# Performance work log

Hardware: AMD Instinct MI355X
Metric: run time of the kernel (lower is better)

The kernel has to match this reference:

```python
import jax, jax.numpy as jnp
import numpy as np

N = 4096        # nodes
D = 512         # in_dim = hidden_dim
E = 131072      # edges (avg degree 32)
K = 3           # aggregate_range
ALPHA = 2.0


def prelu(x, a):
    return jnp.where(x >= 0, x, a * x)


def setup_inputs() -> dict:
    key = jax.random.key(0)
    ks = jax.random.split(key, 8)
    s = 1.0 / np.sqrt(D)  # ~xavier scale
    return {
        "coeffs": jax.random.normal(ks[0], (N, D), jnp.float32),
        "edge_index": jax.random.randint(ks[1], (2, E), 0, N, dtype=jnp.int32),
        "W0": jax.random.normal(ks[2], (D, D), jnp.float32) * s,
        "b0": jnp.zeros((D,), jnp.float32),
        "a0": jnp.full((1,), 0.25, jnp.float32),
        "W1": jax.random.normal(ks[3], (D, D), jnp.float32) * s,  # use_bias=False
        "a1": jnp.full((1,), 0.25, jnp.float32),
        "W2": jax.random.normal(ks[4], (D, D), jnp.float32) * s,
        "a2": jnp.full((1,), 0.25, jnp.float32),
        "Wo": jax.random.normal(ks[5], (1, D), jnp.float32) * s,
        "bo": jnp.zeros((1,), jnp.float32),
    }


def _mlp(coeffs, W0, b0, a0, W1, a1, W2, a2, Wo, bo):
    # Linear+PReLU, then n_hidden_layers x [Linear(no bias)+PReLU+(Dropout: eval, no-op)], then Linear
    x = prelu(coeffs @ W0.T + b0, a0)
    x = prelu(x @ W1.T, a1)
    x = prelu(x @ W2.T, a2)
    return x @ Wo.T + bo  # [N, 1]


def _aggregate_k_hop(edge_index, angles):
    # Faithful to the torch code: enhanced_angles aliases angles, so each hop
    # reads the CURRENT (already enhanced) values:  a <- a + w_k * A_k @ a.
    # Hop 1 uses raw edge list (duplicate edges add twice). Hops >= 2 use
    # np.unique-deduplicated composed paths == boolean adjacency powers.
    src, dst = edge_index[0], edge_index[1]
    a = angles
    a = a + (0.5 ** ALPHA) * jax.ops.segment_sum(a[dst], src, num_segments=N)
    A = jnp.zeros((N, N), jnp.float32).at[src, dst].set(1.0)  # dedup'd boolean adjacency
    Ak = A
    for k_ in range(K - 1):
        Ak = ((Ak @ A) > 0).astype(jnp.float32)  # unique k-hop paths
        a = a + (1.0 / (k_ + 3)) ** ALPHA * (Ak @ a)
    return a


def reference(coeffs, edge_index, W0, b0, a0, W1, a1, W2, a2, Wo, bo):
    angles = _mlp(coeffs, W0, b0, a0, W1, a1, W2, a2, Wo, bo)
    return _aggregate_k_hop(edge_index, angles)
```

## Files before the change

### kernel.cpp

```cpp
#include <hip/hip_runtime.h>

#define N_NODES 4096
#define D_DIM   512
#define E_EDGES 131072
#define NWORDS  128

typedef __bf16 bf16;
typedef __bf16 bf16x4 __attribute__((ext_vector_type(4)));
typedef __bf16 bf16x8 __attribute__((ext_vector_type(8)));
typedef float  f32x4  __attribute__((ext_vector_type(4)));
typedef unsigned int u32;

#define GLOAD_LDS16(gp, lp) \
    __builtin_amdgcn_global_load_lds((const __attribute__((address_space(1))) u32*)(gp), \
                                     (__attribute__((address_space(3))) u32*)(lp), 16, 0, 0)

static const size_t OFF_W1B = 0;
static const size_t OFF_W2B = OFF_W1B + (size_t)D_DIM*D_DIM*2;
static const size_t OFF_X1  = OFF_W2B + (size_t)D_DIM*D_DIM*2;
static const size_t OFF_X2  = OFF_X1  + (size_t)N_NODES*D_DIM*2;
static const size_t OFF_ANG = OFF_X2  + (size_t)N_NODES*D_DIM*2;
static const size_t OFF_H1  = OFF_ANG + N_NODES*4;
static const size_t OFF_A2V = OFF_H1  + N_NODES*4;
static const size_t OFF_TP  = OFF_A2V + N_NODES*4;
static const size_t OFF_AB  = OFF_TP  + 1024*4;
static const size_t OFF_A2B = OFF_AB  + (size_t)N_NODES*NWORDS*4;
static const size_t OFF_A3B = OFF_A2B + (size_t)N_NODES*NWORDS*4;

__device__ __forceinline__ bf16x8 cvt8(float4 lo, float4 hi) {
    bf16x8 r;
    r[0] = (bf16)lo.x; r[1] = (bf16)lo.y; r[2] = (bf16)lo.z; r[3] = (bf16)lo.w;
    r[4] = (bf16)hi.x; r[5] = (bf16)hi.y; r[6] = (bf16)hi.z; r[7] = (bf16)hi.w;
    return r;
}

template<int MODE>
__global__ __launch_bounds__(256)
void gemm_fused(const float* __restrict__ Xf, const float* __restrict__ Wf,
                const bf16* __restrict__ X, const bf16* __restrict__ W,
                bf16* __restrict__ outB,
                const float* __restrict__ bias, const float* __restrict__ slope,
                const float* __restrict__ Wo, float* __restrict__ ang,
                const float* __restrict__ bo, float* __restrict__ h1,
                const float* __restrict__ W1f, const float* __restrict__ W2f,
                bf16* __restrict__ W1b, bf16* __restrict__ W2b,
                const int* __restrict__ esrc, const int* __restrict__ edst,
                u32* __restrict__ AbOut,
                const u32* __restrict__ P, const u32* __restrict__ Q, u32* __restrict__ BOut)
{
    __shared__ bf16 At[2][64][64];
    __shared__ bf16 Bt[2][64][64];
    __shared__ int  s_cnt[4];
    __shared__ int  s_list[4][256];
    const int bx = blockIdx.x;
    const int t = threadIdx.x;
    const int wave = t >> 6, lane = t & 63;

    if (bx < 512) {
        const int wm = wave >> 1, wn = wave & 1;
        const int quad = lane >> 4, lq = lane & 15;
        const int rowBase = (bx >> 3) * 64;
        const int colBase = (bx & 7) * 64;
        const int c0 = t, c1 = t + 256;
        const int r0 = c0 >> 3, o0 = (c0 & 7) * 8;
        const int r1 = c1 >> 3, o1 = (c1 & 7) * 8;

        f32x4 acc[2][2] = {};
        int cur = 0;

        if (MODE == 0) {
            const float* gA0 = Xf + (size_t)(rowBase + r0) * D_DIM + o0;
            const float* gA1 = Xf + (size_t)(rowBase + r1) * D_DIM + o1;
            const float* gB0 = Wf + (size_t)(colBase + r0) * D_DIM + o0;
            const float* gB1 = Wf + (size_t)(colBase + r1) * D_DIM + o1;
            float4 pa0l = *(const float4*)(gA0),     pa0h = *(const float4*)(gA0 + 4);
            float4 pa1l = *(const float4*)(gA1),     pa1h = *(const float4*)(gA1 + 4);
            float4 pb0l = *(const float4*)(gB0),     pb0h = *(const float4*)(gB0 + 4);
            float4 pb1l = *(const float4*)(gB1),     pb1h = *(const float4*)(gB1 + 4);
            for (int k0 = 0; k0 < D_DIM; k0 += 64) {
                *(bf16x8*)&At[cur][r0][o0] = cvt8(pa0l, pa0h);
                *(bf16x8*)&At[cur][r1][o1] = cvt8(pa1l, pa1h);
                *(bf16x8*)&Bt[cur][r0][o0] = cvt8(pb0l, pb0h);
                *(bf16x8*)&Bt[cur][r1][o1] = cvt8(pb1l, pb1h);
                if (k0 + 64 < D_DIM) {
                    pa0l = *(const float4*)(gA0 + k0 + 64); pa0h = *(const float4*)(gA0 + k0 + 68);
                    pa1l = *(const float4*)(gA1 + k0 + 64); pa1h = *(const float4*)(gA1 + k0 + 68);
                    pb0l = *(const float4*)(gB0 + k0 + 64); pb0h = *(const float4*)(gB0 + k0 + 68);
                    pb1l = *(const float4*)(gB1 + k0 + 64); pb1h = *(const float4*)(gB1 + k0 + 68);
                }
                __syncthreads();
                #pragma unroll
                for (int kc = 0; kc < 2; ++kc) {
                    bf16x8 af[2], bfr[2];
                    #pragma unroll
                    for (int tm = 0; tm < 2; ++tm) af[tm]  = *(const bf16x8*)&At[cur][wm * 32 + tm * 16 + lq][kc * 32 + quad * 8];
                    #pragma unroll
                    for (int tn = 0; tn < 2; ++tn) bfr[tn] = *(const bf16x8*)&Bt[cur][wn * 32 + tn * 16 + lq][kc * 32 + quad * 8];
                    #pragma unroll
                    for (int tm = 0; tm < 2; ++tm)
                        #pragma unroll
                        for (int tn = 0; tn < 2; ++tn)
                            acc[tm][tn] = __builtin_amdgcn_mfma_f32_16x16x32_bf16(af[tm], bfr[tn], acc[tm][tn], 0, 0, 0);
                }
                cur ^= 1;
            }
        } else {
            const bf16* gA0 = X + (size_t)(rowBase + r0) * D_DIM + o0;
            const bf16* gA1 = X + (size_t)(rowBase + r1) * D_DIM + o1;
            const bf16* gB0 = W + (size_t)(colBase + r0) * D_DIM + o0;
            const bf16* gB1 = W + (size_t)(colBase + r1) * D_DIM + o1;
            char* baseA = (char*)&At[0][0][0];
            char* baseB = (char*)&Bt[0][0][0];
            GLOAD_LDS16(gA0, baseA + wave * 1024);
            GLOAD_LDS16(gA1, baseA + 4096 + wave * 1024);
            GLOAD_LDS16(gB0, baseB + wave * 1024);
            GLOAD_LDS16(gB1, baseB + 4096 + wave * 1024);
            for (int k0 = 0; k0 < D_DIM; k0 += 64) {
                __syncthreads();
                if (k0 + 64 < D_DIM) {
                    int nb = (cur ^ 1) * 8192;
                    GLOAD_LDS16(gA0 + k0 + 64, baseA + nb + wave * 1024);
                    GLOAD_LDS16(gA1 + k0 + 64, baseA + nb + 4096 + wave * 1024);
                    GLOAD_LDS16(gB0 + k0 + 64, baseB + nb + wave * 1024);
                    GLOAD_LDS16(gB1 + k0 + 64, baseB + nb + 4096 + wave * 1024);
                }
                #pragma unroll
                for (int kc = 0; kc < 2; ++kc) {
                    bf16x8 af[2], bfr[2];
                    #pragma unroll
                    for (int tm = 0; tm < 2; ++tm) af[tm]  = *(const bf16x8*)&At[cur][wm * 32 + tm * 16 + lq][kc * 32 + quad * 8];
                    #pragma unroll
                    for (int tn = 0; tn < 2; ++tn) bfr[tn] = *(const bf16x8*)&Bt[cur][wn * 32 + tn * 16 + lq][kc * 32 + quad * 8];
                    #pragma unroll
                    for (int tm = 0; tm < 2; ++tm)
                        #pragma unroll
                        for (int tn = 0; tn < 2; ++tn)
                            acc[tm][tn] = __builtin_amdgcn_mfma_f32_16x16x32_bf16(af[tm], bfr[tn], acc[tm][tn], 0, 0, 0);
                }
                cur ^= 1;
            }
        }

        const float a = slope[0];
        if (MODE == 2) {
            float wo[2];
            #pragma unroll
            for (int tn = 0; tn < 2; ++tn) wo[tn] = Wo[colBase + wn * 32 + tn * 16 + lq];
            #pragma unroll
            for (int tm = 0; tm < 2; ++tm) {
                #pragma unroll
                for (int r = 0; r < 4; ++r) {
                    float p = 0.f;
                    #pragma unroll
                    for (int tn = 0; tn < 2; ++tn) {
                        float v = acc[tm][tn][r];
                        v = (v >= 0.f) ? v : a * v;
                        p += v * wo[tn];
                    }
                    #pragma unroll
                    for (int m = 1; m < 16; m <<= 1) p += __shfl_xor(p, m, 64);
                    if (lq == 0)
                        atomicAdd(&ang[rowBase + wm * 32 + tm * 16 + quad * 4 + r], p);
                }
            }
        } else {
            #pragma unroll
            for (int tm = 0; tm < 2; ++tm) {
                #pragma unroll
                for (int tn = 0; tn < 2; ++tn) {
                    int col = colBase + wn * 32 + tn * 16 + lq;
                    float b = (MODE == 0) ? bias[col] : 0.f;
                    #pragma unroll
                    for (int r = 0; r < 4; ++r) {
                        int row = rowBase + wm * 32 + tm * 16 + quad * 4 + r;
                        float v = acc[tm][tn][r] + b;
                        v = (v >= 0.f) ? v : a * v;
                        outB[(size_t)row * D_DIM + col] = (bf16)v;
                    }
                }
            }
        }
    } else if (MODE == 0) {
        if (bx < 640) {
            int base = (bx - 512) * 256 + t;
            for (int e = base; e < E_EDGES; e += 128 * 256) {
                int r = esrc[e], c = edst[e];
                atomicOr(&AbOut[(size_t)r * NWORDS + (c >> 5)], 1u << (c & 31));
            }
        } else if (bx < 768) {
            int cb = bx - 640;
            const float* src = (cb < 64) ? W1f : W2f;
            bf16* dst = (cb < 64) ? W1b : W2b;
            size_t base = (size_t)(cb & 63) * 4096;
            #pragma unroll
            for (int i = 0; i < 4; ++i) {
                size_t e = base + (size_t)(i * 256 + t) * 4;
                float4 v = *(const float4*)(src + e);
                bf16x4 o; o.x = (bf16)v.x; o.y = (bf16)v.y; o.z = (bf16)v.z; o.w = (bf16)v.w;
                *(bf16x4*)(dst + e) = o;
            }
        } else {
            float b = bo[0];
            for (int i = t; i < N_NODES; i += 256) { ang[i] = b; h1[i] = 0.f; }
        }
    } else {
        int row = (bx - 512) * 4 + wave;
        if (lane == 0) s_cnt[wave] = 0;
        __syncthreads();
        const u32* prow = P + (size_t)row * NWORDS;
        #pragma unroll
        for (int h = 0; h < 2; ++h) {
            u32 bits = prow[h * 64 + lane];
            int base = (h * 64 + lane) * 32;
            while (bits) {
                int b = __ffs(bits) - 1; bits &= bits - 1;
                int pos = atomicAdd(&s_cnt[wave], 1);
                if (pos < 256) s_list[wave][pos] = base + b;
            }
        }
        __syncthreads();
        int cnt = min(s_cnt[wave], 256);
        u32 acc0 = 0, acc1 = 0;
        int j = 0;
        for (; j + 4 <= cnt; j += 4) {
            int i0 = s_list[wave][j], i1 = s_list[wave][j + 1];
            int i2 = s_list[wave][j + 2], i3 = s_list[wave][j + 3];
            const u32* q0 = Q + (size_t)i0 * NWORDS;
            const u32* q1 = Q + (size_t)i1 * NWORDS;
            const u32* q2 = Q + (size_t)i2 * NWORDS;
            const u32* q3 = Q + (size_t)i3 * NWORDS;
            u32 x0 = q0[lane], x1 = q1[lane], x2 = q2[lane], x3 = q3[lane];
            u32 y0 = q0[64 + lane], y1 = q1[64 + lane], y2 = q2[64 + lane], y3 = q3[64 + lane];
            acc0 |= x0 | x1 | x2 | x3;
            acc1 |= y0 | y1 | y2 | y3;
        }
        for (; j < cnt; ++j) {
            const u32* q = Q + (size_t)s_list[wave][j] * NWORDS;
            acc0 |= q[lane]; acc1 |= q[64 + lane];
        }
        BOut[(size_t)row * NWORDS + lane]      = acc0;
        BOut[(size_t)row * NWORDS + 64 + lane] = acc1;
    }
}

__global__ __launch_bounds__(256)
void hop1_edges(const int* __restrict__ src, const int* __restrict__ dst,
                const float* __restrict__ ang, float* __restrict__ h1)
{
    int e = blockIdx.x * 256 + threadIdx.x;
    if (e < E_EDGES) atomicAdd(&h1[src[e]], 0.25f * ang[dst[e]]);
}

__global__ __launch_bounds__(256)
void bits_matvec2(const u32* __restrict__ A2, const float* __restrict__ ang,
                  const float* __restrict__ h1, float* __restrict__ a2,
                  float* __restrict__ Tpart)
{
    __shared__ float s_red[4];
    int wave = threadIdx.x >> 6, lane = threadIdx.x & 63;
    int row  = blockIdx.x * 4 + wave;
    float s = 0.f;
    #pragma unroll
    for (int h = 0; h < 2; ++h) {
        u32 bits = A2[(size_t)row * NWORDS + h * 64 + lane];
        int base = (h * 64 + lane) * 32;
        while (bits) {
            int b = __ffs(bits) - 1;
            bits &= bits - 1;
            s += ang[base + b] + h1[base + b];
        }
    }
    #pragma unroll
    for (int off = 32; off > 0; off >>= 1) s += __shfl_down(s, off, 64);
    if (lane == 0) {
        float val = (ang[row] + h1[row]) + (1.f / 9.f) * s;
        a2[row] = val;
        s_red[wave] = val;
    }
    __syncthreads();
    if (threadIdx.x == 0)
        Tpart[blockIdx.x] = s_red[0] + s_red[1] + s_red[2] + s_red[3];
}

__global__ __launch_bounds__(256)
void bits_matvec3(const u32* __restrict__ A3, const float* __restrict__ a2,
                  const float* __restrict__ Tpart, float* __restrict__ out)
{
    __shared__ float s_part[4];
    int wave = threadIdx.x >> 6, lane = threadIdx.x & 63;

    float tsum = 0.f;
    #pragma unroll
    for (int i = 0; i < 4; ++i) tsum += Tpart[i * 256 + threadIdx.x];
    #pragma unroll
    for (int off = 32; off > 0; off >>= 1) tsum += __shfl_down(tsum, off, 64);
    if (lane == 0) s_part[wave] = tsum;
    __syncthreads();
    const float T = s_part[0] + s_part[1] + s_part[2] + s_part[3];

    int row = blockIdx.x * 4 + wave;
    float s = 0.f;
    #pragma unroll
    for (int h = 0; h < 2; ++h) {
        u32 bits = ~A3[(size_t)row * NWORDS + h * 64 + lane];
        int base = (h * 64 + lane) * 32;
        while (bits) {
            int b = __ffs(bits) - 1;
            bits &= bits - 1;
            s += a2[base + b];
        }
    }
    #pragma unroll
    for (int off = 32; off > 0; off >>= 1) s += __shfl_down(s, off, 64);
    if (lane == 0) out[row] = a2[row] + (1.f / 16.f) * (T - s);
}

extern "C" void kernel_launch(void* const* d_in, const int* in_sizes, int n_in,
                              void* d_out, int out_size, void* d_ws, size_t ws_size,
                              hipStream_t stream) {
    const float* coeffs = (const float*)d_in[0];
    const int*   edges  = (const int*)d_in[1];
    const float* W0     = (const float*)d_in[2];
    const float* b0     = (const float*)d_in[3];
    const float* pa0    = (const float*)d_in[4];
    const float* W1     = (const float*)d_in[5];
    const float* pa1    = (const float*)d_in[6];
    const float* W2     = (const float*)d_in[7];
    const float* pa2    = (const float*)d_in[8];
    const float* Wo     = (const float*)d_in[9];
    const float* bo     = (const float*)d_in[10];
    float* out = (float*)d_out;

    char* ws = (char*)d_ws;
    bf16*  W1b  = (bf16*)(ws + OFF_W1B);
    bf16*  W2b  = (bf16*)(ws + OFF_W2B);
    bf16*  x1b  = (bf16*)(ws + OFF_X1);
    bf16*  x2b  = (bf16*)(ws + OFF_X2);
    float* ang  = (float*)(ws + OFF_ANG);
    float* h1   = (float*)(ws + OFF_H1);
    float* a2v  = (float*)(ws + OFF_A2V);
    float* Tp   = (float*)(ws + OFF_TP);
    u32*   Ab   = (u32*)(ws + OFF_AB);
    u32*   A2b  = (u32*)(ws + OFF_A2B);
    u32*   A3b  = (u32*)(ws + OFF_A3B);

    const int* srcp = edges;
    const int* dstp = edges + E_EDGES;

    hipMemsetAsync(Ab, 0, (size_t)N_NODES * NWORDS * 4, stream);

    gemm_fused<0><<<769, 256, 0, stream>>>(coeffs, W0, nullptr, nullptr, x1b, b0, pa0,
                                           nullptr, ang, bo, h1, W1, W2, W1b, W2b,
                                           srcp, dstp, Ab, nullptr, nullptr, nullptr);
    gemm_fused<1><<<1536, 256, 0, stream>>>(nullptr, nullptr, x1b, W1b, x2b, nullptr, pa1,
                                            nullptr, nullptr, nullptr, nullptr, nullptr, nullptr,
                                            nullptr, nullptr, nullptr, nullptr, nullptr, Ab, Ab, A2b);
    gemm_fused<2><<<1536, 256, 0, stream>>>(nullptr, nullptr, x2b, W2b, nullptr, nullptr, pa2,
                                            Wo, ang, nullptr, nullptr, nullptr, nullptr, nullptr, nullptr,
                                            nullptr, nullptr, nullptr, Ab, A2b, A3b);

    hop1_edges<<<E_EDGES / 256, 256, 0, stream>>>(srcp, dstp, ang, h1);
    bits_matvec2<<<N_NODES / 4, 256, 0, stream>>>(A2b, ang, h1, a2v, Tp);
    bits_matvec3<<<N_NODES / 4, 256, 0, stream>>>(A3b, a2v, Tp, out);
}
```

Baseline: 146.8 us.

## Fuse hop1 and two bitmask matvecs into one kernel with grid barriers

Replaces the three small aggregation kernels (edge atomics, hop-2 and hop-3 bit matvecs) with a single persistent kernel of 1024 blocks that separates the phases with software grid barriers built on atomic counters. The barrier counters are zeroed by the existing memset, which is extended to cover them. The goal is to remove two kernel launch gaps and their tail effects. The cost is spin-wait barrier latency, and the kernel relies on all 1024 blocks being resident at once to avoid deadlock.

```diff
diff --git a/kernel.cpp b/kernel.cpp
--- a/kernel.cpp
+++ b/kernel.cpp
@@ -4,6 +4,7 @@
 #define D_DIM   512
 #define E_EDGES 131072
 #define NWORDS  128
+#define AGG_BLOCKS 1024
 
 typedef __bf16 bf16;
 typedef __bf16 bf16x4 __attribute__((ext_vector_type(4)));
@@ -23,7 +24,9 @@
 static const size_t OFF_H1  = OFF_ANG + N_NODES*4;
 static const size_t OFF_A2V = OFF_H1  + N_NODES*4;
 static const size_t OFF_TP  = OFF_A2V + N_NODES*4;
-static const size_t OFF_AB  = OFF_TP  + 1024*4;
+static const size_t OFF_CTR = OFF_TP  + 1024*4;
+static const size_t OFF_AB  = OFF_CTR + 256;
+static const size_t ZERO_BYTES = 256 + (size_t)N_NODES*NWORDS*4;
 static const size_t OFF_A2B = OFF_AB  + (size_t)N_NODES*NWORDS*4;
 static const size_t OFF_A3B = OFF_A2B + (size_t)N_NODES*NWORDS*4;
 
@@ -32,6 +35,19 @@
     r[0] = (bf16)lo.x; r[1] = (bf16)lo.y; r[2] = (bf16)lo.z; r[3] = (bf16)lo.w;
     r[4] = (bf16)hi.x; r[5] = (bf16)hi.y; r[6] = (bf16)hi.z; r[7] = (bf16)hi.w;
     return r;
+}
+
+__device__ __forceinline__ void grid_barrier(u32* cnt) {
+    __syncthreads();
+    if (threadIdx.x == 0) {
+        __threadfence();
+        u32 arrived = atomicAdd(cnt, 1u) + 1;
+        while (arrived < AGG_BLOCKS) {
+            __builtin_amdgcn_s_sleep(1);
+            arrived = atomicAdd(cnt, 0u);
+        }
+    }
+    __syncthreads();
 }
 
 template<int MODE>
@@ -244,75 +260,73 @@
 }
 
 __global__ __launch_bounds__(256)
-void hop1_edges(const int* __restrict__ src, const int* __restrict__ dst,
-                const float* __restrict__ ang, float* __restrict__ h1)
-{
-    int e = blockIdx.x * 256 + threadIdx.x;
-    if (e < E_EDGES) atomicAdd(&h1[src[e]], 0.25f * ang[dst[e]]);
-}
-
-__global__ __launch_bounds__(256)
-void bits_matvec2(const u32* __restrict__ A2, const float* __restrict__ ang,
-                  const float* __restrict__ h1, float* __restrict__ a2,
-                  float* __restrict__ Tpart)
+void aggregate(const int* __restrict__ esrc, const int* __restrict__ edst,
+               const float* __restrict__ ang, float* __restrict__ h1,
+               const u32* __restrict__ A2, const u32* __restrict__ A3,
+               float* __restrict__ a2v, float* __restrict__ Tp,
+               u32* __restrict__ ctr, float* __restrict__ out)
 {
     __shared__ float s_red[4];
-    int wave = threadIdx.x >> 6, lane = threadIdx.x & 63;
-    int row  = blockIdx.x * 4 + wave;
-    float s = 0.f;
-    #pragma unroll
-    for (int h = 0; h < 2; ++h) {
-        u32 bits = A2[(size_t)row * NWORDS + h * 64 + lane];
-        int base = (h * 64 + lane) * 32;
-        while (bits) {
-            int b = __ffs(bits) - 1;
-            bits &= bits - 1;
-            s += ang[base + b] + h1[base + b];
-        }
-    }
-    #pragma unroll
-    for (int off = 32; off > 0; off >>= 1) s += __shfl_down(s, off, 64);
-    if (lane == 0) {
-        float val = (ang[row] + h1[row]) + (1.f / 9.f) * s;
-        a2[row] = val;
-        s_red[wave] = val;
-    }
-    __syncthreads();
-    if (threadIdx.x == 0)
-        Tpart[blockIdx.x] = s_red[0] + s_red[1] + s_red[2] + s_red[3];
-}
-
-__global__ __launch_bounds__(256)
-void bits_matvec3(const u32* __restrict__ A3, const float* __restrict__ a2,
-                  const float* __restrict__ Tpart, float* __restrict__ out)
-{
-    __shared__ float s_part[4];
-    int wave = threadIdx.x >> 6, lane = threadIdx.x & 63;
-
-    float tsum = 0.f;
-    #pragma unroll
-    for (int i = 0; i < 4; ++i) tsum += Tpart[i * 256 + threadIdx.x];
-    #pragma unroll
-    for (int off = 32; off > 0; off >>= 1) tsum += __shfl_down(tsum, off, 64);
-    if (lane == 0) s_part[wave] = tsum;
-    __syncthreads();
-    const float T = s_part[0] + s_part[1] + s_part[2] + s_part[3];
-
-    int row = blockIdx.x * 4 + wave;
-    float s = 0.f;
-    #pragma unroll
-    for (int h = 0; h < 2; ++h) {
-        u32 bits = ~A3[(size_t)row * NWORDS + h * 64 + lane];
-        int base = (h * 64 + lane) * 32;
-        while (bits) {
-            int b = __ffs(bits) - 1;
-            bits &= bits - 1;
-            s += a2[base + b];
-        }
-    }
-    #pragma unroll
-    for (int off = 32; off > 0; off >>= 1) s += __shfl_down(s, off, 64);
-    if (lane == 0) out[row] = a2[row] + (1.f / 16.f) * (T - s);
+    const int bx = blockIdx.x;
+    const int t = threadIdx.x;
+    const int wave = t >> 6, lane = t & 63;
+
+    if (t < 128) {
+        int e = bx * 128 + t;
+        atomicAdd(&h1[esrc[e]], 0.25f * ang[edst[e]]);
+    }
+    grid_barrier(&ctr[0]);
+
+    {
+        int row = bx * 4 + wave;
+        float s = 0.f;
+        #pragma unroll
+        for (int h = 0; h < 2; ++h) {
+            u32 bits = A2[(size_t)row * NWORDS + h * 64 + lane];
+            int base = (h * 64 + lane) * 32;
+            while (bits) {
+                int b = __ffs(bits) - 1; bits &= bits - 1;
+                s += ang[base + b] + h1[base + b];
+            }
+        }
+        #pragma unroll
+        for (int off = 32; off > 0; off >>= 1) s += __shfl_down(s, off, 64);
+        if (lane == 0) {
+            float val = (ang[row] + h1[row]) + (1.f / 9.f) * s;
+            a2v[row] = val;
+            s_red[wave] = val;
+        }
+        __syncthreads();
+        if (t == 0) Tp[bx] = s_red[0] + s_red[1] + s_red[2] + s_red[3];
+    }
+    grid_barrier(&ctr[16]);
+
+    {
+        float tsum = 0.f;
+        #pragma unroll
+        for (int i = 0; i < 4; ++i) tsum += Tp[i * 256 + t];
+        #pragma unroll
+        for (int off = 32; off > 0; off >>= 1) tsum += __shfl_down(tsum, off, 64);
+        __syncthreads();
+        if (lane == 0) s_red[wave] = tsum;
+        __syncthreads();
+        const float T = s_red[0] + s_red[1] + s_red[2] + s_red[3];
+
+        int row = bx * 4 + wave;
+        float s = 0.f;
+        #pragma unroll
+        for (int h = 0; h < 2; ++h) {
+            u32 bits = ~A3[(size_t)row * NWORDS + h * 64 + lane];
+            int base = (h * 64 + lane) * 32;
+            while (bits) {
+                int b = __ffs(bits) - 1; bits &= bits - 1;
+                s += a2v[base + b];
+            }
+        }
+        #pragma unroll
+        for (int off = 32; off > 0; off >>= 1) s += __shfl_down(s, off, 64);
+        if (lane == 0) out[row] = a2v[row] + (1.f / 16.f) * (T - s);
+    }
 }
 
 extern "C" void kernel_launch(void* const* d_in, const int* in_sizes, int n_in,
@@ -340,6 +354,7 @@
     float* h1   = (float*)(ws + OFF_H1);
     float* a2v  = (float*)(ws + OFF_A2V);
     float* Tp   = (float*)(ws + OFF_TP);
+    u32*   ctr  = (u32*)(ws + OFF_CTR);
     u32*   Ab   = (u32*)(ws + OFF_AB);
     u32*   A2b  = (u32*)(ws + OFF_A2B);
     u32*   A3b  = (u32*)(ws + OFF_A3B);
@@ -347,7 +362,7 @@
     const int* srcp = edges;
     const int* dstp = edges + E_EDGES;
 
-    hipMemsetAsync(Ab, 0, (size_t)N_NODES * NWORDS * 4, stream);
+    hipMemsetAsync(ws + OFF_CTR, 0, ZERO_BYTES, stream);
 
     gemm_fused<0><<<769, 256, 0, stream>>>(coeffs, W0, nullptr, nullptr, x1b, b0, pa0,
                                            nullptr, ang, bo, h1, W1, W2, W1b, W2b,
@@ -359,7 +374,5 @@
                                             Wo, ang, nullptr, nullptr, nullptr, nullptr, nullptr, nullptr,
                                             nullptr, nullptr, nullptr, Ab, A2b, A3b);
 
-    hop1_edges<<<E_EDGES / 256, 256, 0, stream>>>(srcp, dstp, ang, h1);
-    bits_matvec2<<<N_NODES / 4, 256, 0, stream>>>(A2b, ang, h1, a2v, Tp);
-    bits_matvec3<<<N_NODES / 4, 256, 0, stream>>>(A3b, a2v, Tp, out);
-}
+    aggregate<<<AGG_BLOCKS, 256, 0, stream>>>(srcp, dstp, ang, h1, A2b, A3b, a2v, Tp, ctr, out);
+}
```

After: 252.7 us. 1.72x slower.
